# Kernel tuning notes

Hardware: AMD Instinct MI355X
Metric: run time of the kernel (lower is better)

Reference implementation:

```python
import jax, jax.numpy as jnp
import numpy as np
import math

T_STEPS = 100      # diffusion steps
TED = 16           # time_embed_dim
NODE_C = 4         # node_num_classes
EDGE_C = 2         # edge_num_classes
HID = 64           # hidden_dim
H = 4              # nhead
B = 256            # graphs per batch
NPG = 64           # nodes per graph
DEG = 8            # avg out-degree
N = B * NPG
E = N * DEG
IN_CH = NODE_C + TED  # 20


def sinusoidal_embedding(t_vec, dim):
    # t_vec: [1] float. Matches get_sinusoidal_embedding for even dim.
    half = dim // 2
    scale = math.log(10000.0) / (half - 1)
    freqs = jnp.exp(-jnp.arange(half, dtype=jnp.float32) * scale)  # [half]
    emb = t_vec[:, None] * freqs[None, :]                          # [1, half]
    return jnp.concatenate([jnp.sin(emb), jnp.cos(emb)], axis=1)   # [1, dim]


def transformer_conv(x, src, dst, Wq, bq, Wk, bk, Wv, bv, Ws, bs):
    # PyG TransformerConv, concat=False (mean over heads), root_weight=True,
    # beta=False, no edge features, dropout=0 (eval).
    n = x.shape[0]
    q = (x @ Wq + bq).reshape(n, H, HID)
    k = (x @ Wk + bk).reshape(n, H, HID)
    v = (x @ Wv + bv).reshape(n, H, HID)
    # attention logits per edge, softmax over incoming edges of each dst node
    logits = jnp.sum(q[dst] * k[src], axis=-1) / math.sqrt(HID)    # [E, H]
    lmax = jax.ops.segment_max(logits, dst, num_segments=n)       # [n, H]
    ex = jnp.exp(logits - lmax[dst])                              # [E, H]
    denom = jax.ops.segment_sum(ex, dst, num_segments=n)          # [n, H]
    attn = ex / jnp.where(denom == 0, 1.0, denom)[dst]            # [E, H]
    msg = v[src] * attn[:, :, None]                               # [E, H, HID]
    agg = jax.ops.segment_sum(msg, dst, num_segments=n)           # [n, H, HID]
    return agg.mean(axis=1) + x @ Ws + bs                         # [n, HID]


def setup_inputs() -> dict:
    key = jax.random.key(0)
    ks = jax.random.split(key, 32)

    # node features: random one-hot labels
    labels = jax.random.randint(ks[0], (N,), 0, NODE_C)
    x = jax.nn.one_hot(labels, NODE_C, dtype=jnp.float32)

    # per-graph random edges (kept within each graph via offsets)
    src_l = jax.random.randint(ks[1], (B, NPG * DEG), 0, NPG)
    dst_l = jax.random.randint(ks[2], (B, NPG * DEG), 0, NPG)
    off = (jnp.arange(B) * NPG)[:, None]
    edge_index = jnp.stack([(src_l + off).reshape(-1), (dst_l + off).reshape(-1)]).astype(jnp.int64)

    batch = jnp.repeat(jnp.arange(B, dtype=jnp.int64), NPG)

    def lin(k, fin, fout):
        kw, kb = jax.random.split(k)
        W = jax.random.normal(kw, (fin, fout), jnp.float32) / math.sqrt(fin)
        b = jax.random.normal(kb, (fout,), jnp.float32) * 0.01
        return W, b

    W_time, b_time = lin(ks[3], TED, TED)
    Wq1, bq1 = lin(ks[4], IN_CH, H * HID)
    Wk1, bk1 = lin(ks[5], IN_CH, H * HID)
    Wv1, bv1 = lin(ks[6], IN_CH, H * HID)
    Ws1, bs1 = lin(ks[7], IN_CH, HID)
    Wq2, bq2 = lin(ks[8], HID, H * HID)
    Wk2, bk2 = lin(ks[9], HID, H * HID)
    Wv2, bv2 = lin(ks[10], HID, H * HID)
    Ws2, bs2 = lin(ks[11], HID, HID)
    W_node, b_node = lin(ks[12], HID, NODE_C)
    W_e1, b_e1 = lin(ks[13], 2 * HID, HID)
    W_e2, b_e2 = lin(ks[14], HID, EDGE_C)

    return dict(x=x, edge_index=edge_index, batch=batch, t=50,
                W_time=W_time, b_time=b_time,
                Wq1=Wq1, bq1=bq1, Wk1=Wk1, bk1=bk1, Wv1=Wv1, bv1=bv1, Ws1=Ws1, bs1=bs1,
                Wq2=Wq2, bq2=bq2, Wk2=Wk2, bk2=bk2, Wv2=Wv2, bv2=bv2, Ws2=Ws2, bs2=bs2,
                W_node=W_node, b_node=b_node, W_e1=W_e1, b_e1=b_e1, W_e2=W_e2, b_e2=b_e2)


def reference(x, edge_index, batch, t,
              W_time, b_time,
              Wq1, bq1, Wk1, bk1, Wv1, bv1, Ws1, bs1,
              Wq2, bq2, Wk2, bk2, Wv2, bv2, Ws2, bs2,
              W_node, b_node, W_e1, b_e1, W_e2, b_e2):
    src, dst = edge_index[0], edge_index[1]

    # time embedding: sinusoidal(t/T) -> Linear -> broadcast to all nodes
    t_vec = jnp.asarray([t], jnp.float32) / T_STEPS
    temb = sinusoidal_embedding(t_vec, TED) @ W_time + b_time      # [1, TED]
    temb = jnp.broadcast_to(temb, (x.shape[0], TED))
    x_in = jnp.concatenate([x, temb], axis=1)                      # [N, 20]

    h = jax.nn.relu(transformer_conv(x_in, src, dst, Wq1, bq1, Wk1, bk1, Wv1, bv1, Ws1, bs1))
    h = jax.nn.relu(transformer_conv(h, src, dst, Wq2, bq2, Wk2, bk2, Wv2, bv2, Ws2, bs2))

    node_logits = h @ W_node + b_node                              # [N, 4]

    # to_dense_batch with equal-sized graphs == reshape; vectorized edge MLP
    hd = h.reshape(B, NPG, HID)
    pair = jnp.concatenate([
        jnp.broadcast_to(hd[:, :, None, :], (B, NPG, NPG, HID)),
        jnp.broadcast_to(hd[:, None, :, :], (B, NPG, NPG, HID)),
    ], axis=-1)                                                    # [B, n, n, 2*HID]
    e_hidden = jax.nn.relu(pair @ W_e1 + b_e1)
    edge_logits = e_hidden @ W_e2 + b_e2                           # [B, n, n, 2]
    return node_logits, edge_logits
```

## Files before the change

kernel.cpp:

```cpp
#include <hip/hip_runtime.h>
#include <math.h>

constexpr int EPG  = 512;
constexpr int ETOT = 131072;

constexpr size_t TAB_Q  = 0;
constexpr size_t TAB_K  = 1024;
constexpr size_t TAB_V  = 2048;
constexpr size_t TAB_S  = 3072;
constexpr size_t TAB_LG = 3328;
constexpr size_t OFF_H2 = 65536;
constexpr int PK_Q_HI   = 0;
constexpr int PK_Q_LO   = 16384;
constexpr int PK_K_HI   = 32768;
constexpr int PK_K_LO   = 49152;
constexpr int PK_V_HI   = 65536;
constexpr int PK_V_LO   = 81920;
constexpr int PK_S_HI   = 98304;
constexpr int PK_S_LO   = 102400;
constexpr int PK_E1T_HI = 106496;
constexpr int PK_E1T_LO = 110592;
constexpr int PK_E1B_HI = 114688;
constexpr int PK_E1B_LO = 118784;

typedef short bf16x8 __attribute__((ext_vector_type(8)));
typedef float f32x4  __attribute__((ext_vector_type(4)));

__device__ __forceinline__ short f2bf(float x) {
    unsigned u = __float_as_uint(x);
    u = (u + 0x7fffu + ((u >> 16) & 1u)) >> 16;
    return (short)u;
}
__device__ __forceinline__ float bf2f(short h) {
    return __uint_as_float(((unsigned)(unsigned short)h) << 16);
}
__device__ __forceinline__ void splt(float x, short& hi, short& lo) {
    hi = f2bf(x);
    lo = f2bf(x - bf2f(hi));
}

__device__ __forceinline__ f32x4 mfma3(bf16x8 ah, bf16x8 al, bf16x8 bh, bf16x8 bl, f32x4 c) {
    c = __builtin_amdgcn_mfma_f32_16x16x32_bf16(ah, bh, c, 0, 0, 0);
    c = __builtin_amdgcn_mfma_f32_16x16x32_bf16(ah, bl, c, 0, 0, 0);
    c = __builtin_amdgcn_mfma_f32_16x16x32_bf16(al, bh, c, 0, 0, 0);
    return c;
}

__device__ __forceinline__ bf16x8 ldsfrag(const short* p, int rowb, int kb, int lane) {
    return *(const bf16x8*)&p[(rowb + (lane & 15)) * 72 + kb + ((lane >> 4) << 3)];
}
__device__ __forceinline__ bf16x8 gpfrag(const short* p, int colb, int kb, int lane) {
    return *(const bf16x8*)&p[((colb + (lane & 15)) << 6) + kb + ((lane >> 4) << 3)];
}

__device__ __forceinline__ void unpack8(const unsigned* p, bf16x8& hv, bf16x8& lv) {
    uint4 a = *(const uint4*)p;
    uint4 b = *(const uint4*)(p + 4);
    unsigned u[8] = {a.x, a.y, a.z, a.w, b.x, b.y, b.z, b.w};
    bf16x8 h, l;
    #pragma unroll
    for (int i = 0; i < 8; i++) { h[i] = (short)(u[i] >> 16); l[i] = (short)(u[i] & 0xffffu); }
    hv = h; lv = l;
}

__global__ __launch_bounds__(256) void k_tabprep(
    const int* __restrict__ t_ptr,
    const float* __restrict__ Wt,  const float* __restrict__ bt,
    const float* __restrict__ Wq1, const float* __restrict__ bq1,
    const float* __restrict__ Wk1, const float* __restrict__ bk1,
    const float* __restrict__ Wv1, const float* __restrict__ bv1,
    const float* __restrict__ Ws1, const float* __restrict__ bs1,
    const float* __restrict__ Wq2, const float* __restrict__ Wk2,
    const float* __restrict__ Wv2, const float* __restrict__ Ws2,
    const float* __restrict__ We1,
    float* __restrict__ ws, short* __restrict__ wsh)
{
    const int t = threadIdx.x;
    if (blockIdx.x < 240) {
        int b = blockIdx.x;
        const float* src; int N; int dhi; int nb;
        if (b < 64)       { src = Wq2;           N = 256; dhi = PK_Q_HI;   nb = b; }
        else if (b < 128) { src = Wk2;           N = 256; dhi = PK_K_HI;   nb = b - 64; }
        else if (b < 192) { src = Wv2;           N = 256; dhi = PK_V_HI;   nb = b - 128; }
        else if (b < 208) { src = Ws2;           N = 64;  dhi = PK_S_HI;   nb = b - 192; }
        else if (b < 224) { src = We1;           N = 64;  dhi = PK_E1T_HI; nb = b - 208; }
        else              { src = We1 + 64 * 64; N = 64;  dhi = PK_E1B_HI; nb = b - 224; }
        int dlo = dhi + N * 64;
        int n = nb * 4 + (t >> 6), kk = t & 63;
        float v = src[(size_t)kk * N + n];
        short hi, lo; splt(v, hi, lo);
        wsh[dhi + n * 64 + kk] = hi;
        wsh[dlo + n * 64 + kk] = lo;
        return;
    }
    __shared__ float se[16], temb[16];
    __shared__ float q1t[4][256], k1t[4][256], v1t[4][256], s1t[4][64];
    if (t < 8) {
        float tv = (float)(*t_ptr) * 0.01f;
        float scale = logf(10000.0f) / 7.0f;
        float e = tv * expf(-(float)t * scale);
        se[t]     = sinf(e);
        se[t + 8] = cosf(e);
    }
    __syncthreads();
    if (t < 16) {
        float acc = bt[t];
        for (int i = 0; i < 16; i++) acc += se[i] * Wt[i * 16 + t];
        temb[t] = acc;
    }
    __syncthreads();
    {
        const int o = t;
        float tq = 0.f, tk = 0.f, tv = 0.f;
        for (int d = 0; d < 16; d++) {
            float td = temb[d];
            tq += td * Wq1[(4 + d) * 256 + o];
            tk += td * Wk1[(4 + d) * 256 + o];
            tv += td * Wv1[(4 + d) * 256 + o];
        }
        for (int c = 0; c < 4; c++) {
            q1t[c][o] = Wq1[c * 256 + o] + tq + bq1[o];
            k1t[c][o] = Wk1[c * 256 + o] + tk + bk1[o];
            v1t[c][o] = Wv1[c * 256 + o] + tv + bv1[o];
        }
        if (o < 64) {
            float ts = 0.f;
            for (int d = 0; d < 16; d++) ts += temb[d] * Ws1[(4 + d) * 64 + o];
            for (int c = 0; c < 4; c++) s1t[c][o] = Ws1[c * 64 + o] + ts + bs1[o];
        }
    }
    __syncthreads();
    for (int idx = t; idx < 1024; idx += 256) {
        int c = idx >> 8, o = idx & 255;
        ws[TAB_Q + idx] = q1t[c][o];
        ws[TAB_K + idx] = k1t[c][o];
        ws[TAB_V + idx] = v1t[c][o];
    }
    ws[TAB_S + t] = s1t[t >> 6][t & 63];
    if (t < 64) {
        int cd = t >> 4, cs = (t >> 2) & 3, h = t & 3;
        float acc = 0.f;
        for (int d = 0; d < 64; d++) acc += q1t[cd][h * 64 + d] * k1t[cs][h * 64 + d];
        ws[TAB_LG + t] = acc * 0.125f;
    }
}

__global__ __launch_bounds__(512, 4) void k_main(
    const float* __restrict__ x, const int* __restrict__ ei,
    const float* __restrict__ ws, const short* __restrict__ wsh,
    const float* __restrict__ bq, const float* __restrict__ bk,
    const float* __restrict__ bv, const float* __restrict__ bsk,
    float* __restrict__ h2out)
{
    __shared__ __align__(16) char smem[78976];
    short* hHi  = (short*)(smem);
    short* hLo  = (short*)(smem + 9216);
    short* kHi  = (short*)(smem + 18432);
    short* kLo  = (short*)(smem + 27648);
    short* vtHi = (short*)(smem + 36864);
    short* vtLo = (short*)(smem + 46080);
    short* qHi  = (short*)(smem + 55296);
    short* qLo  = (short*)(smem + 59904);
    float* SPf  = (float*)(smem + 64512);
    unsigned* SPu = (unsigned*)(smem + 64512);
    int*   Cc   = (int*)(smem + 73216);
    int*   cnt4 = (int*)(smem + 77312);
    int*   cls  = (int*)(smem + 78336);
    float* lgs  = (float*)(smem + 78592);
    float* invs = (float*)(smem + 78848);
    float* v1t    = (float*)(smem + 18432);
    float* s1t    = (float*)(smem + 22528);
    float* alphaF = (float*)(smem + 23552);

    const int g   = blockIdx.x >> 1;
    const int r0  = (blockIdx.x & 1) * 32;
    const int t   = threadIdx.x;
    const int lane = t & 63, w = t >> 6;
    const int rowbF = (w & 3) * 16;
    const int chF   = w >> 2;
    const int rbQ   = (w & 1) * 16;
    const int cqQ   = (w >> 1) * 16;
    const int lg4   = ((lane >> 4) << 2);
    const int l15   = lane & 15;
    const int row8  = t >> 3;
    const int d08   = (t & 7) * 8;

    for (int i = t; i < 1024; i += 512) v1t[i] = ws[TAB_V + i];
    if (t < 256) s1t[t] = ws[TAB_S + t];
    if (t < 64)  lgs[t] = ws[TAB_LG + t];
    if (t < 64) {
        const float* xr = x + (size_t)(g * 64 + t) * 4;
        int c = 0;
        if (xr[1] > 0.5f) c = 1;
        if (xr[2] > 0.5f) c = 2;
        if (xr[3] > 0.5f) c = 3;
        cls[t] = c;
    }
    if (t < 256) cnt4[t] = 0;
    for (int i = t; i < 1024; i += 512) Cc[i] = 0;
    __syncthreads();

    {
        int ge = g * EPG + t;
        int ls = ei[ge] - g * 64;
        int ld = ei[ETOT + ge] - g * 64;
        atomicAdd(&cnt4[ld * 4 + cls[ls]], 1);
        int lr = ld - r0;
        if ((unsigned)lr < 32u) {
            int idx = lr * 64 + ls;
            atomicAdd(&Cc[idx >> 1], 1 << ((idx & 1) * 16));
        }
    }
    __syncthreads();

    if (t < 256) {
        int n = t >> 2, h = t & 3;
        int cd = cls[n];
        int   c[4]; float l[4];
        #pragma unroll
        for (int cc = 0; cc < 4; cc++) {
            c[cc] = cnt4[n * 4 + cc];
            l[cc] = lgs[cd * 16 + cc * 4 + h];
        }
        float m = -1e30f;
        #pragma unroll
        for (int cc = 0; cc < 4; cc++) if (c[cc] > 0) m = fmaxf(m, l[cc]);
        float e[4]; float den = 0.f;
        #pragma unroll
        for (int cc = 0; cc < 4; cc++) {
            e[cc] = (c[cc] > 0) ? (float)c[cc] * expf(l[cc] - m) : 0.f;
            den += e[cc];
        }
        float inv = (den > 0.f) ? 0.25f / den : 0.f;
        #pragma unroll
        for (int cc = 0; cc < 4; cc++) alphaF[n * 16 + h * 4 + cc] = e[cc] * inv;
    }
    __syncthreads();

    {
        int cd = cls[row8];
        float a[16];
        #pragma unroll
        for (int q = 0; q < 16; q++) a[q] = alphaF[row8 * 16 + q];
        #pragma unroll
        for (int jj = 0; jj < 8; jj++) {
            int d = d08 + jj;
            float acc = s1t[cd * 64 + d];
            #pragma unroll
            for (int h = 0; h < 4; h++)
                #pragma unroll
                for (int c = 0; c < 4; c++)
                    acc += a[h * 4 + c] * v1t[c * 256 + h * 64 + d];
            float o = fmaxf(acc, 0.f);
            short hi, lo; splt(o, hi, lo);
            hHi[row8 * 72 + d] = hi;
            hLo[row8 * 72 + d] = lo;
        }
    }
    __syncthreads();

    bf16x8 AhF0 = ldsfrag(hHi, rowbF, 0, lane),     AhF1 = ldsfrag(hHi, rowbF, 32, lane);
    bf16x8 AlF0 = ldsfrag(hLo, rowbF, 0, lane),     AlF1 = ldsfrag(hLo, rowbF, 32, lane);
    bf16x8 AhQ0 = ldsfrag(hHi, r0 + rbQ, 0, lane),  AhQ1 = ldsfrag(hHi, r0 + rbQ, 32, lane);
    bf16x8 AlQ0 = ldsfrag(hLo, r0 + rbQ, 0, lane),  AlQ1 = ldsfrag(hLo, r0 + rbQ, 32, lane);

    f32x4 skacc;
    {
        f32x4 a = {0.f, 0.f, 0.f, 0.f};
        a = mfma3(AhQ0, AlQ0, gpfrag(wsh + PK_S_HI, cqQ, 0, lane),
                               gpfrag(wsh + PK_S_LO, cqQ, 0, lane), a);
        a = mfma3(AhQ1, AlQ1, gpfrag(wsh + PK_S_HI, cqQ, 32, lane),
                               gpfrag(wsh + PK_S_LO, cqQ, 32, lane), a);
        float bb = bsk[cqQ + l15];
        #pragma unroll
        for (int r = 0; r < 4; r++) a[r] += bb;
        skacc = a;
    }

    float hacc[4] = {0.f, 0.f, 0.f, 0.f};
    #pragma unroll 1
    for (int h = 0; h < 4; h++) {
        #pragma unroll
        for (int ct = 0; ct < 2; ct++) {
            int colb = chF * 32 + ct * 16;
            int gcol = h * 64 + colb;
            f32x4 ka = {0.f, 0.f, 0.f, 0.f}, va = {0.f, 0.f, 0.f, 0.f};
            ka = mfma3(AhF0, AlF0, gpfrag(wsh + PK_K_HI, gcol, 0, lane),
                                    gpfrag(wsh + PK_K_LO, gcol, 0, lane), ka);
            ka = mfma3(AhF1, AlF1, gpfrag(wsh + PK_K_HI, gcol, 32, lane),
                                    gpfrag(wsh + PK_K_LO, gcol, 32, lane), ka);
            va = mfma3(AhF0, AlF0, gpfrag(wsh + PK_V_HI, gcol, 0, lane),
                                    gpfrag(wsh + PK_V_LO, gcol, 0, lane), va);
            va = mfma3(AhF1, AlF1, gpfrag(wsh + PK_V_HI, gcol, 32, lane),
                                    gpfrag(wsh + PK_V_LO, gcol, 32, lane), va);
            float bkv = bk[gcol + l15];
            float bvv = bv[gcol + l15];
            int cc = colb + l15;
            #pragma unroll
            for (int r = 0; r < 4; r++) {
                int rr = rowbF + lg4 + r;
                short hi, lo;
                splt(ka[r] + bkv, hi, lo);
                kHi[rr * 72 + cc] = hi;  kLo[rr * 72 + cc] = lo;
                splt(va[r] + bvv, hi, lo);
                vtHi[cc * 72 + rr] = hi; vtLo[cc * 72 + rr] = lo;
            }
        }
        {
            int gcol = h * 64 + cqQ;
            f32x4 qa = {0.f, 0.f, 0.f, 0.f};
            qa = mfma3(AhQ0, AlQ0, gpfrag(wsh + PK_Q_HI, gcol, 0, lane),
                                    gpfrag(wsh + PK_Q_LO, gcol, 0, lane), qa);
            qa = mfma3(AhQ1, AlQ1, gpfrag(wsh + PK_Q_HI, gcol, 32, lane),
                                    gpfrag(wsh + PK_Q_LO, gcol, 32, lane), qa);
            float bqv = bq[gcol + l15];
            int cc = cqQ + l15;
            #pragma unroll
            for (int r = 0; r < 4; r++) {
                int rr = rbQ + lg4 + r;
                short hi, lo;
                splt((qa[r] + bqv) * 0.125f, hi, lo);
                qHi[rr * 72 + cc] = hi;  qLo[rr * 72 + cc] = lo;
            }
        }
        __syncthreads();

        {
            bf16x8 qh0 = ldsfrag(qHi, rbQ, 0, lane),  qh1 = ldsfrag(qHi, rbQ, 32, lane);
            bf16x8 ql0 = ldsfrag(qLo, rbQ, 0, lane),  ql1 = ldsfrag(qLo, rbQ, 32, lane);
            f32x4 s = {0.f, 0.f, 0.f, 0.f};
            s = mfma3(qh0, ql0, ldsfrag(kHi, cqQ, 0, lane),
                                 ldsfrag(kLo, cqQ, 0, lane), s);
            s = mfma3(qh1, ql1, ldsfrag(kHi, cqQ, 32, lane),
                                 ldsfrag(kLo, cqQ, 32, lane), s);
            int cc = cqQ + l15;
            #pragma unroll
            for (int r = 0; r < 4; r++)
                SPf[(rbQ + lg4 + r) * 68 + cc] = s[r];
        }
        __syncthreads();

        if (t < 256) {
            int row = t >> 3, c8 = (t & 7) * 8;
            float4 s0 = *(float4*)&SPf[row * 68 + c8];
            float4 s1 = *(float4*)&SPf[row * 68 + c8 + 4];
            float sv[8] = {s0.x, s0.y, s0.z, s0.w, s1.x, s1.y, s1.z, s1.w};
            int cv[8];
            #pragma unroll
            for (int jj = 0; jj < 8; jj++) {
                int idx = row * 64 + c8 + jj;
                cv[jj] = (Cc[idx >> 1] >> ((idx & 1) * 16)) & 0xffff;
            }
            float m = -1e30f;
            #pragma unroll
            for (int jj = 0; jj < 8; jj++) if (cv[jj] > 0) m = fmaxf(m, sv[jj]);
            m = fmaxf(m, __shfl_xor(m, 1, 8));
            m = fmaxf(m, __shfl_xor(m, 2, 8));
            m = fmaxf(m, __shfl_xor(m, 4, 8));
            float den = 0.f; float p[8];
            #pragma unroll
            for (int jj = 0; jj < 8; jj++) {
                p[jj] = (cv[jj] > 0) ? (float)cv[jj] * expf(sv[jj] - m) : 0.f;
                den += p[jj];
            }
            den += __shfl_xor(den, 1, 8);
            den += __shfl_xor(den, 2, 8);
            den += __shfl_xor(den, 4, 8);
            #pragma unroll
            for (int jj = 0; jj < 8; jj++) {
                short hi, lo; splt(p[jj], hi, lo);
                SPu[row * 68 + c8 + jj] =
                    ((unsigned)(unsigned short)hi << 16) | (unsigned short)lo;
            }
            if ((t & 7) == 0) invs[row] = (den > 0.f) ? 1.f / den : 0.f;
        }
        __syncthreads();

        {
            bf16x8 ph0, pl0, ph1, pl1;
            const unsigned* pp = SPu + (rbQ + l15) * 68 + ((lane >> 4) << 3);
            unpack8(pp, ph0, pl0);
            unpack8(pp + 32, ph1, pl1);
            f32x4 pv = {0.f, 0.f, 0.f, 0.f};
            pv = mfma3(ph0, pl0, ldsfrag(vtHi, cqQ, 0, lane),
                                  ldsfrag(vtLo, cqQ, 0, lane), pv);
            pv = mfma3(ph1, pl1, ldsfrag(vtHi, cqQ, 32, lane),
                                  ldsfrag(vtLo, cqQ, 32, lane), pv);
            #pragma unroll
            for (int r = 0; r < 4; r++)
                hacc[r] += pv[r] * invs[rbQ + lg4 + r];
        }
        __syncthreads();
    }

    {
        int cc = cqQ + l15;
        #pragma unroll
        for (int r = 0; r < 4; r++) {
            int lr = rbQ + lg4 + r;
            float v = fmaxf(0.25f * hacc[r] + skacc[r], 0.f);
            h2out[(size_t)(g * 64 + r0 + lr) * 64 + cc] = v;
        }
    }
}

__global__ __launch_bounds__(512, 4) void k_edge(
    const short* __restrict__ wsh, const float* __restrict__ h2g,
    const float* __restrict__ Wn, const float* __restrict__ bn,
    const float* __restrict__ be1, const float* __restrict__ We2,
    const float* __restrict__ be2, float* __restrict__ out)
{
    __shared__ __align__(16) char smem[46080];
    short* h2Hi = (short*)(smem);
    short* h2Lo = (short*)(smem + 9216);
    float* Af   = (float*)(smem + 18432);
    float* BTf  = (float*)(smem + 27136);
    float* WnS  = (float*)(smem + 44544);
    float* w2s  = (float*)(smem + 45568);

    const int g  = blockIdx.x >> 1;
    const int r0 = (blockIdx.x & 1) * 32;
    const int t  = threadIdx.x;
    const int lane = t & 63, w = t >> 6;
    const int rowbF = (w & 3) * 16, chF = w >> 2;
    const int rbQ = (w & 1) * 16,   cqQ = (w >> 1) * 16;
    const int lg4 = ((lane >> 4) << 2);
    const int l15 = lane & 15;

    {
        int row = t >> 3, c8 = (t & 7) * 8;
        float4 a = *(const float4*)&h2g[(size_t)(g * 64 + row) * 64 + c8];
        float4 b = *(const float4*)&h2g[(size_t)(g * 64 + row) * 64 + c8 + 4];
        float vv[8] = {a.x, a.y, a.z, a.w, b.x, b.y, b.z, b.w};
        #pragma unroll
        for (int i = 0; i < 8; i++) {
            short hi, lo; splt(vv[i], hi, lo);
            h2Hi[row * 72 + c8 + i] = hi;
            h2Lo[row * 72 + c8 + i] = lo;
        }
    }
    if (t < 256) WnS[t] = Wn[t];
    if (t < 128) w2s[(t & 1) * 64 + (t >> 1)] = We2[t];
    __syncthreads();

    {
        bf16x8 aq0 = ldsfrag(h2Hi, r0 + rbQ, 0, lane), aq1 = ldsfrag(h2Hi, r0 + rbQ, 32, lane);
        bf16x8 lq0 = ldsfrag(h2Lo, r0 + rbQ, 0, lane), lq1 = ldsfrag(h2Lo, r0 + rbQ, 32, lane);
        f32x4 aa = {0.f, 0.f, 0.f, 0.f};
        aa = mfma3(aq0, lq0, gpfrag(wsh + PK_E1T_HI, cqQ, 0, lane),
                              gpfrag(wsh + PK_E1T_LO, cqQ, 0, lane), aa);
        aa = mfma3(aq1, lq1, gpfrag(wsh + PK_E1T_HI, cqQ, 32, lane),
                              gpfrag(wsh + PK_E1T_LO, cqQ, 32, lane), aa);
        float bev = be1[cqQ + l15];
        #pragma unroll
        for (int r = 0; r < 4; r++)
            Af[(rbQ + lg4 + r) * 68 + cqQ + l15] = aa[r] + bev;

        bf16x8 af0 = ldsfrag(h2Hi, rowbF, 0, lane), af1 = ldsfrag(h2Hi, rowbF, 32, lane);
        bf16x8 lf0 = ldsfrag(h2Lo, rowbF, 0, lane), lf1 = ldsfrag(h2Lo, rowbF, 32, lane);
        #pragma unroll
        for (int ct = 0; ct < 2; ct++) {
            int colb = chF * 32 + ct * 16;
            f32x4 bb = {0.f, 0.f, 0.f, 0.f};
            bb = mfma3(af0, lf0, gpfrag(wsh + PK_E1B_HI, colb, 0, lane),
                                  gpfrag(wsh + PK_E1B_LO, colb, 0, lane), bb);
            bb = mfma3(af1, lf1, gpfrag(wsh + PK_E1B_HI, colb, 32, lane),
                                  gpfrag(wsh + PK_E1B_LO, colb, 32, lane), bb);
            int cc = colb + l15;
            #pragma unroll
            for (int r = 0; r < 4; r++)
                BTf[cc * 68 + rowbF + lg4 + r] = bb[r];
        }
    }
    if (t < 128) {
        int n = t >> 2, c = t & 3;
        float acc = bn[c];
        #pragma unroll 4
        for (int k = 0; k < 64; k++)
            acc += (bf2f(h2Hi[(r0 + n) * 72 + k]) + bf2f(h2Lo[(r0 + n) * 72 + k])) * WnS[k * 4 + c];
        out[(size_t)(g * 64 + r0 + n) * 4 + c] = acc;
    }
    __syncthreads();

    {
        const int wv = t >> 6, j = t & 63;
        float e0[4], e1[4];
        const float cb0 = be2[0], cb1 = be2[1];
        #pragma unroll
        for (int ii = 0; ii < 4; ii++) { e0[ii] = cb0; e1[ii] = cb1; }
        for (int kb = 0; kb < 4; kb++) {
            const int k0 = kb * 16;
            float bj[16], wa[16], wb[16];
            #pragma unroll
            for (int q = 0; q < 16; q++) {
                bj[q] = BTf[(k0 + q) * 68 + j];
                wa[q] = w2s[k0 + q];
                wb[q] = w2s[64 + k0 + q];
            }
            #pragma unroll
            for (int ii = 0; ii < 4; ii++) {
                const float* ar = &Af[(wv * 4 + ii) * 68 + k0];
                #pragma unroll
                for (int q = 0; q < 16; q += 4) {
                    float4 a4 = *(const float4*)(ar + q);
                    float s;
                    s = fmaxf(a4.x + bj[q + 0], 0.f); e0[ii] += s * wa[q + 0]; e1[ii] += s * wb[q + 0];
                    s = fmaxf(a4.y + bj[q + 1], 0.f); e0[ii] += s * wa[q + 1]; e1[ii] += s * wb[q + 1];
                    s = fmaxf(a4.z + bj[q + 2], 0.f); e0[ii] += s * wa[q + 2]; e1[ii] += s * wb[q + 2];
                    s = fmaxf(a4.w + bj[q + 3], 0.f); e0[ii] += s * wa[q + 3]; e1[ii] += s * wb[q + 3];
                }
            }
        }
        float2* oe = (float2*)(out + 65536);
        #pragma unroll
        for (int ii = 0; ii < 4; ii++)
            oe[(size_t)(g * 64 + r0 + wv * 4 + ii) * 64 + j] = make_float2(e0[ii], e1[ii]);
    }
}

extern "C" void kernel_launch(void* const* d_in, const int* in_sizes, int n_in,
                              void* d_out, int out_size, void* d_ws, size_t ws_size,
                              hipStream_t stream)
{
    const float* x    = (const float*)d_in[0];
    const int*   ei   = (const int*)d_in[1];
    const int*   tptr = (const int*)d_in[3];
    const float* Wt   = (const float*)d_in[4];
    const float* bt   = (const float*)d_in[5];
    const float* Wq1  = (const float*)d_in[6];
    const float* bq1  = (const float*)d_in[7];
    const float* Wk1  = (const float*)d_in[8];
    const float* bk1  = (const float*)d_in[9];
    const float* Wv1  = (const float*)d_in[10];
    const float* bv1  = (const float*)d_in[11];
    const float* Ws1  = (const float*)d_in[12];
    const float* bs1  = (const float*)d_in[13];
    const float* Wq2  = (const float*)d_in[14];
    const float* bq2  = (const float*)d_in[15];
    const float* Wk2  = (const float*)d_in[16];
    const float* bk2  = (const float*)d_in[17];
    const float* Wv2  = (const float*)d_in[18];
    const float* bv2  = (const float*)d_in[19];
    const float* Ws2  = (const float*)d_in[20];
    const float* bs2  = (const float*)d_in[21];
    const float* Wn   = (const float*)d_in[22];
    const float* bn   = (const float*)d_in[23];
    const float* We1  = (const float*)d_in[24];
    const float* be1  = (const float*)d_in[25];
    const float* We2  = (const float*)d_in[26];
    const float* be2  = (const float*)d_in[27];

    float* ws  = (float*)d_ws;
    short* wsh = (short*)(ws + 4096);
    float* h2  = ws + OFF_H2;
    float* out = (float*)d_out;

    k_tabprep<<<241, 256, 0, stream>>>(tptr, Wt, bt, Wq1, bq1, Wk1, bk1, Wv1, bv1,
                                       Ws1, bs1, Wq2, Wk2, Wv2, Ws2, We1, ws, wsh);
    k_main<<<512, 512, 0, stream>>>(x, ei, ws, wsh, bq2, bk2, bv2, bs2, h2);
    k_edge<<<512, 512, 0, stream>>>(wsh, h2, Wn, bn, be1, We2, be2, out);
}
```

Measured before the change: 76.29 us.

## Fold Wq·Wkᵀ into a per-head bilinear matrix and pass h2 as packed bf16 pairs

Layer-2 attention logits are now computed as (h·M_h)·hᵀ, where M_h = Wq_h·Wk_hᵀ/8 is precomputed per head in the prep kernel. Because the key bias only adds a per-row constant, which softmax cancels, it is dropped, and the query-bias term folds into a per-column vector. This removes the per-block K projection and lets the softmax run on MFMA fragments in registers, cutting LDS traffic and shared memory. h2 is stored as packed hi/lo bf16 words so the edge kernel no longer has to re-split it, and expf is swapped for __expf, at some risk to accuracy.

```diff
diff --git a/kernel.cpp b/kernel.cpp
--- a/kernel.cpp
+++ b/kernel.cpp
@@ -9,19 +9,19 @@
 constexpr size_t TAB_V  = 2048;
 constexpr size_t TAB_S  = 3072;
 constexpr size_t TAB_LG = 3328;
-constexpr size_t OFF_H2 = 65536;
-constexpr int PK_Q_HI   = 0;
-constexpr int PK_Q_LO   = 16384;
-constexpr int PK_K_HI   = 32768;
-constexpr int PK_K_LO   = 49152;
-constexpr int PK_V_HI   = 65536;
-constexpr int PK_V_LO   = 81920;
-constexpr int PK_S_HI   = 98304;
-constexpr int PK_S_LO   = 102400;
-constexpr int PK_E1T_HI = 106496;
-constexpr int PK_E1T_LO = 110592;
-constexpr int PK_E1B_HI = 114688;
-constexpr int PK_E1B_LO = 118784;
+constexpr size_t TAB_VV = 3392;
+constexpr size_t OFF_H2P = 65536;
+
+constexpr int PK_V_HI   = 0;
+constexpr int PK_V_LO   = 16384;
+constexpr int PK_S_HI   = 32768;
+constexpr int PK_S_LO   = 36864;
+constexpr int PK_E1T_HI = 40960;
+constexpr int PK_E1T_LO = 45056;
+constexpr int PK_E1B_HI = 49152;
+constexpr int PK_E1B_LO = 53248;
+constexpr int PK_M_HI   = 57344;
+constexpr int PK_M_LO   = 73728;
 
 typedef short bf16x8 __attribute__((ext_vector_type(8)));
 typedef float f32x4  __attribute__((ext_vector_type(4)));
@@ -70,27 +70,49 @@
     const float* __restrict__ Wk1, const float* __restrict__ bk1,
     const float* __restrict__ Wv1, const float* __restrict__ bv1,
     const float* __restrict__ Ws1, const float* __restrict__ bs1,
-    const float* __restrict__ Wq2, const float* __restrict__ Wk2,
-    const float* __restrict__ Wv2, const float* __restrict__ Ws2,
-    const float* __restrict__ We1,
+    const float* __restrict__ Wq2, const float* __restrict__ bq2,
+    const float* __restrict__ Wk2, const float* __restrict__ Wv2,
+    const float* __restrict__ Ws2, const float* __restrict__ We1,
     float* __restrict__ ws, short* __restrict__ wsh)
 {
-    const int t = threadIdx.x;
-    if (blockIdx.x < 240) {
-        int b = blockIdx.x;
+    const int t = threadIdx.x, b = blockIdx.x;
+    if (b < 112) {
         const float* src; int N; int dhi; int nb;
-        if (b < 64)       { src = Wq2;           N = 256; dhi = PK_Q_HI;   nb = b; }
-        else if (b < 128) { src = Wk2;           N = 256; dhi = PK_K_HI;   nb = b - 64; }
-        else if (b < 192) { src = Wv2;           N = 256; dhi = PK_V_HI;   nb = b - 128; }
-        else if (b < 208) { src = Ws2;           N = 64;  dhi = PK_S_HI;   nb = b - 192; }
-        else if (b < 224) { src = We1;           N = 64;  dhi = PK_E1T_HI; nb = b - 208; }
-        else              { src = We1 + 64 * 64; N = 64;  dhi = PK_E1B_HI; nb = b - 224; }
+        if (b < 64)      { src = Wv2;           N = 256; dhi = PK_V_HI;   nb = b; }
+        else if (b < 80) { src = Ws2;           N = 64;  dhi = PK_S_HI;   nb = b - 64; }
+        else if (b < 96) { src = We1;           N = 64;  dhi = PK_E1T_HI; nb = b - 80; }
+        else             { src = We1 + 64 * 64; N = 64;  dhi = PK_E1B_HI; nb = b - 96; }
         int dlo = dhi + N * 64;
         int n = nb * 4 + (t >> 6), kk = t & 63;
         float v = src[(size_t)kk * N + n];
         short hi, lo; splt(v, hi, lo);
         wsh[dhi + n * 64 + kk] = hi;
         wsh[dlo + n * 64 + kk] = lo;
+        return;
+    }
+    if (b < 116) {
+        int h = b - 112;
+        __shared__ float wq[64][65], wk[64][65];
+        for (int i = t; i < 4096; i += 256) {
+            int r = i >> 6, a = i & 63;
+            wq[r][a] = Wq2[(size_t)r * 256 + h * 64 + a];
+            wk[r][a] = Wk2[(size_t)r * 256 + h * 64 + a];
+        }
+        __syncthreads();
+        int m = t >> 2, k0 = (t & 3) * 16;
+        for (int kk = k0; kk < k0 + 16; kk++) {
+            float acc = 0.f;
+            for (int a = 0; a < 64; a++) acc += wq[kk][a] * wk[m][a];
+            acc *= 0.125f;
+            short hi, lo; splt(acc, hi, lo);
+            wsh[PK_M_HI + h * 4096 + m * 64 + kk] = hi;
+            wsh[PK_M_LO + h * 4096 + m * 64 + kk] = lo;
+        }
+        if (t < 64) {
+            float acc = 0.f;
+            for (int a = 0; a < 64; a++) acc += wk[t][a] * bq2[h * 64 + a];
+            ws[TAB_VV + h * 64 + t] = 0.125f * acc;
+        }
         return;
     }
     __shared__ float se[16], temb[16];
@@ -148,46 +170,45 @@
 __global__ __launch_bounds__(512, 4) void k_main(
     const float* __restrict__ x, const int* __restrict__ ei,
     const float* __restrict__ ws, const short* __restrict__ wsh,
-    const float* __restrict__ bq, const float* __restrict__ bk,
     const float* __restrict__ bv, const float* __restrict__ bsk,
-    float* __restrict__ h2out)
+    unsigned* __restrict__ h2p)
 {
-    __shared__ __align__(16) char smem[78976];
+    __shared__ __align__(16) char smem[61184];
     short* hHi  = (short*)(smem);
     short* hLo  = (short*)(smem + 9216);
-    short* kHi  = (short*)(smem + 18432);
-    short* kLo  = (short*)(smem + 27648);
-    short* vtHi = (short*)(smem + 36864);
-    short* vtLo = (short*)(smem + 46080);
-    short* qHi  = (short*)(smem + 55296);
-    short* qLo  = (short*)(smem + 59904);
-    float* SPf  = (float*)(smem + 64512);
-    unsigned* SPu = (unsigned*)(smem + 64512);
-    int*   Cc   = (int*)(smem + 73216);
-    int*   cnt4 = (int*)(smem + 77312);
-    int*   cls  = (int*)(smem + 78336);
-    float* lgs  = (float*)(smem + 78592);
-    float* invs = (float*)(smem + 78848);
-    float* v1t    = (float*)(smem + 18432);
-    float* s1t    = (float*)(smem + 22528);
-    float* alphaF = (float*)(smem + 23552);
+    short* GHi  = (short*)(smem + 18432);
+    short* GLo  = (short*)(smem + 23040);
+    short* VtHi = (short*)(smem + 27648);
+    short* VtLo = (short*)(smem + 36864);
+    float* SPf  = (float*)(smem + 46080);
+    int*   Cc   = (int*)(smem + 54784);
+    float* wcol = (float*)(smem + 59136);
+    float* vvs  = (float*)(smem + 60160);
+    float* v1t    = (float*)(smem + 27648);
+    float* s1t    = (float*)(smem + 31744);
+    float* lgs    = (float*)(smem + 32768);
+    float* alphaF = (float*)(smem + 33024);
+    int*   cls    = (int*)(smem + 37120);
+    int*   cnt4   = (int*)(smem + 37376);
 
     const int g   = blockIdx.x >> 1;
     const int r0  = (blockIdx.x & 1) * 32;
     const int t   = threadIdx.x;
     const int lane = t & 63, w = t >> 6;
-    const int rowbF = (w & 3) * 16;
-    const int chF   = w >> 2;
-    const int rbQ   = (w & 1) * 16;
-    const int cqQ   = (w >> 1) * 16;
-    const int lg4   = ((lane >> 4) << 2);
-    const int l15   = lane & 15;
-    const int row8  = t >> 3;
-    const int d08   = (t & 7) * 8;
+    const int rb  = (w & 1) * 16;
+    const int cb  = (w >> 1) * 16;
+    const int db  = (w & 3) * 16;
+    const int jb0 = (w >> 2) * 32;
+    const int lg4 = ((lane >> 4) << 2);
+    const int lg8 = ((lane >> 4) << 3);
+    const int l15 = lane & 15;
+    const int row8 = t >> 3;
+    const int d08  = (t & 7) * 8;
 
     for (int i = t; i < 1024; i += 512) v1t[i] = ws[TAB_V + i];
     if (t < 256) s1t[t] = ws[TAB_S + t];
     if (t < 64)  lgs[t] = ws[TAB_LG + t];
+    if (t < 256) vvs[t] = ws[TAB_VV + t];
     if (t < 64) {
         const float* xr = x + (size_t)(g * 64 + t) * 4;
         int c = 0;
@@ -197,7 +218,7 @@
         cls[t] = c;
     }
     if (t < 256) cnt4[t] = 0;
-    for (int i = t; i < 1024; i += 512) Cc[i] = 0;
+    for (int i = t; i < 1056; i += 512) Cc[i] = 0;
     __syncthreads();
 
     {
@@ -207,7 +228,7 @@
         atomicAdd(&cnt4[ld * 4 + cls[ls]], 1);
         int lr = ld - r0;
         if ((unsigned)lr < 32u) {
-            int idx = lr * 64 + ls;
+            int idx = lr * 66 + ls;
             atomicAdd(&Cc[idx >> 1], 1 << ((idx & 1) * 16));
         }
     }
@@ -228,7 +249,7 @@
         float e[4]; float den = 0.f;
         #pragma unroll
         for (int cc = 0; cc < 4; cc++) {
-            e[cc] = (c[cc] > 0) ? (float)c[cc] * expf(l[cc] - m) : 0.f;
+            e[cc] = (c[cc] > 0) ? (float)c[cc] * __expf(l[cc] - m) : 0.f;
             den += e[cc];
         }
         float inv = (den > 0.f) ? 0.25f / den : 0.f;
@@ -259,164 +280,169 @@
     }
     __syncthreads();
 
-    bf16x8 AhF0 = ldsfrag(hHi, rowbF, 0, lane),     AhF1 = ldsfrag(hHi, rowbF, 32, lane);
-    bf16x8 AlF0 = ldsfrag(hLo, rowbF, 0, lane),     AlF1 = ldsfrag(hLo, rowbF, 32, lane);
-    bf16x8 AhQ0 = ldsfrag(hHi, r0 + rbQ, 0, lane),  AhQ1 = ldsfrag(hHi, r0 + rbQ, 32, lane);
-    bf16x8 AlQ0 = ldsfrag(hLo, r0 + rbQ, 0, lane),  AlQ1 = ldsfrag(hLo, r0 + rbQ, 32, lane);
-
-    f32x4 skacc;
-    {
-        f32x4 a = {0.f, 0.f, 0.f, 0.f};
-        a = mfma3(AhQ0, AlQ0, gpfrag(wsh + PK_S_HI, cqQ, 0, lane),
-                               gpfrag(wsh + PK_S_LO, cqQ, 0, lane), a);
-        a = mfma3(AhQ1, AlQ1, gpfrag(wsh + PK_S_HI, cqQ, 32, lane),
-                               gpfrag(wsh + PK_S_LO, cqQ, 32, lane), a);
-        float bb = bsk[cqQ + l15];
-        #pragma unroll
-        for (int r = 0; r < 4; r++) a[r] += bb;
-        skacc = a;
+    bf16x8 AhQ0 = ldsfrag(hHi, r0 + rb, 0, lane),  AhQ1 = ldsfrag(hHi, r0 + rb, 32, lane);
+    bf16x8 AlQ0 = ldsfrag(hLo, r0 + rb, 0, lane),  AlQ1 = ldsfrag(hLo, r0 + rb, 32, lane);
+    bf16x8 sb0h = ldsfrag(hHi, cb, 0, lane),  sb0l = ldsfrag(hLo, cb, 0, lane);
+    bf16x8 sb1h = ldsfrag(hHi, cb, 32, lane), sb1l = ldsfrag(hLo, cb, 32, lane);
+
+    if (t < 256) {
+        int j = t >> 2, hh = t & 3;
+        float acc = 0.f;
+        #pragma unroll 8
+        for (int k = 0; k < 64; k++)
+            acc += (bf2f(hHi[j * 72 + k]) + bf2f(hLo[j * 72 + k])) * vvs[hh * 64 + k];
+        wcol[hh * 64 + j] = acc;
+    }
+
+    f32x4 skacc = {0.f, 0.f, 0.f, 0.f};
+    {
+        bf16x8 s0h = gpfrag(wsh + PK_S_HI, cb, 0, lane),  s0l = gpfrag(wsh + PK_S_LO, cb, 0, lane);
+        bf16x8 s1h = gpfrag(wsh + PK_S_HI, cb, 32, lane), s1l = gpfrag(wsh + PK_S_LO, cb, 32, lane);
+        skacc = mfma3(AhQ0, AlQ0, s0h, s0l, skacc);
+        skacc = mfma3(AhQ1, AlQ1, s1h, s1l, skacc);
+        float bb = bsk[cb + l15];
+        #pragma unroll
+        for (int r = 0; r < 4; r++) skacc[r] += bb;
     }
 
     float hacc[4] = {0.f, 0.f, 0.f, 0.f};
     #pragma unroll 1
     for (int h = 0; h < 4; h++) {
-        #pragma unroll
-        for (int ct = 0; ct < 2; ct++) {
-            int colb = chF * 32 + ct * 16;
-            int gcol = h * 64 + colb;
-            f32x4 ka = {0.f, 0.f, 0.f, 0.f}, va = {0.f, 0.f, 0.f, 0.f};
-            ka = mfma3(AhF0, AlF0, gpfrag(wsh + PK_K_HI, gcol, 0, lane),
-                                    gpfrag(wsh + PK_K_LO, gcol, 0, lane), ka);
-            ka = mfma3(AhF1, AlF1, gpfrag(wsh + PK_K_HI, gcol, 32, lane),
-                                    gpfrag(wsh + PK_K_LO, gcol, 32, lane), ka);
-            va = mfma3(AhF0, AlF0, gpfrag(wsh + PK_V_HI, gcol, 0, lane),
-                                    gpfrag(wsh + PK_V_LO, gcol, 0, lane), va);
-            va = mfma3(AhF1, AlF1, gpfrag(wsh + PK_V_HI, gcol, 32, lane),
-                                    gpfrag(wsh + PK_V_LO, gcol, 32, lane), va);
-            float bkv = bk[gcol + l15];
-            float bvv = bv[gcol + l15];
-            int cc = colb + l15;
+        const short* pmh = wsh + PK_M_HI + h * 4096;
+        const short* pml = wsh + PK_M_LO + h * 4096;
+        bf16x8 m0h = gpfrag(pmh, cb, 0, lane),  m0l = gpfrag(pml, cb, 0, lane);
+        bf16x8 m1h = gpfrag(pmh, cb, 32, lane), m1l = gpfrag(pml, cb, 32, lane);
+        int gc0 = h * 64 + db;
+        bf16x8 va0h = gpfrag(wsh + PK_V_HI, gc0, 0, lane),  va0l = gpfrag(wsh + PK_V_LO, gc0, 0, lane);
+        bf16x8 va1h = gpfrag(wsh + PK_V_HI, gc0, 32, lane), va1l = gpfrag(wsh + PK_V_LO, gc0, 32, lane);
+        float4 bv4 = *(const float4*)&bv[gc0 + lg4];
+        bf16x8 hb00 = ldsfrag(hHi, jb0, 0, lane),       hb00l = ldsfrag(hLo, jb0, 0, lane);
+        bf16x8 hb01 = ldsfrag(hHi, jb0, 32, lane),      hb01l = ldsfrag(hLo, jb0, 32, lane);
+        bf16x8 hb10 = ldsfrag(hHi, jb0 + 16, 0, lane),  hb10l = ldsfrag(hLo, jb0 + 16, 0, lane);
+        bf16x8 hb11 = ldsfrag(hHi, jb0 + 16, 32, lane), hb11l = ldsfrag(hLo, jb0 + 16, 32, lane);
+
+        {
+            f32x4 ga = {0.f, 0.f, 0.f, 0.f};
+            ga = mfma3(AhQ0, AlQ0, m0h, m0l, ga);
+            ga = mfma3(AhQ1, AlQ1, m1h, m1l, ga);
+            int cc = cb + l15;
             #pragma unroll
             for (int r = 0; r < 4; r++) {
-                int rr = rowbF + lg4 + r;
+                short hi, lo; splt(ga[r], hi, lo);
+                GHi[(rb + lg4 + r) * 72 + cc] = hi;
+                GLo[(rb + lg4 + r) * 72 + cc] = lo;
+            }
+        }
+        {
+            f32x4 vt0 = {0.f, 0.f, 0.f, 0.f}, vt1 = {0.f, 0.f, 0.f, 0.f};
+            vt0 = mfma3(va0h, va0l, hb00, hb00l, vt0);
+            vt0 = mfma3(va1h, va1l, hb01, hb01l, vt0);
+            vt1 = mfma3(va0h, va0l, hb10, hb10l, vt1);
+            vt1 = mfma3(va1h, va1l, hb11, hb11l, vt1);
+            #pragma unroll
+            for (int r = 0; r < 4; r++) {
+                int rr = (db + lg4 + r) * 72;
                 short hi, lo;
-                splt(ka[r] + bkv, hi, lo);
-                kHi[rr * 72 + cc] = hi;  kLo[rr * 72 + cc] = lo;
-                splt(va[r] + bvv, hi, lo);
-                vtHi[cc * 72 + rr] = hi; vtLo[cc * 72 + rr] = lo;
-            }
-        }
+                splt(vt0[r] + bv4[r], hi, lo);
+                VtHi[rr + jb0 + l15] = hi;      VtLo[rr + jb0 + l15] = lo;
+                splt(vt1[r] + bv4[r], hi, lo);
+                VtHi[rr + jb0 + 16 + l15] = hi; VtLo[rr + jb0 + 16 + l15] = lo;
+            }
+        }
+        __syncthreads();
+
+        bf16x8 vb0h = ldsfrag(VtHi, cb, 0, lane),  vb0l = ldsfrag(VtLo, cb, 0, lane);
+        bf16x8 vb1h = ldsfrag(VtHi, cb, 32, lane), vb1l = ldsfrag(VtLo, cb, 32, lane);
         {
-            int gcol = h * 64 + cqQ;
-            f32x4 qa = {0.f, 0.f, 0.f, 0.f};
-            qa = mfma3(AhQ0, AlQ0, gpfrag(wsh + PK_Q_HI, gcol, 0, lane),
-                                    gpfrag(wsh + PK_Q_LO, gcol, 0, lane), qa);
-            qa = mfma3(AhQ1, AlQ1, gpfrag(wsh + PK_Q_HI, gcol, 32, lane),
-                                    gpfrag(wsh + PK_Q_LO, gcol, 32, lane), qa);
-            float bqv = bq[gcol + l15];
-            int cc = cqQ + l15;
-            #pragma unroll
-            for (int r = 0; r < 4; r++) {
-                int rr = rbQ + lg4 + r;
+            bf16x8 g0h = ldsfrag(GHi, rb, 0, lane),  g0l = ldsfrag(GLo, rb, 0, lane);
+            bf16x8 g1h = ldsfrag(GHi, rb, 32, lane), g1l = ldsfrag(GLo, rb, 32, lane);
+            f32x4 s = {0.f, 0.f, 0.f, 0.f};
+            s = mfma3(g0h, g0l, sb0h, sb0l, s);
+            s = mfma3(g1h, g1l, sb1h, sb1l, s);
+            int cc = cb + l15;
+            #pragma unroll
+            for (int r = 0; r < 4; r++)
+                SPf[(rb + lg4 + r) * 68 + cc] = s[r];
+        }
+        __syncthreads();
+
+        {
+            const int lr = rb + l15;
+            float sv[16];
+            {
+                float4 a0 = *(const float4*)&SPf[lr * 68 + lg8];
+                float4 a1 = *(const float4*)&SPf[lr * 68 + lg8 + 4];
+                float4 a2 = *(const float4*)&SPf[lr * 68 + 32 + lg8];
+                float4 a3 = *(const float4*)&SPf[lr * 68 + 32 + lg8 + 4];
+                sv[0]=a0.x; sv[1]=a0.y; sv[2]=a0.z; sv[3]=a0.w;
+                sv[4]=a1.x; sv[5]=a1.y; sv[6]=a1.z; sv[7]=a1.w;
+                sv[8]=a2.x; sv[9]=a2.y; sv[10]=a2.z; sv[11]=a2.w;
+                sv[12]=a3.x; sv[13]=a3.y; sv[14]=a3.z; sv[15]=a3.w;
+            }
+            int cv[16];
+            #pragma unroll
+            for (int e = 0; e < 8; e++) {
+                int i0 = lr * 66 + lg8 + e;
+                int i1 = lr * 66 + 32 + lg8 + e;
+                cv[e]     = (Cc[i0 >> 1] >> ((i0 & 1) * 16)) & 0xffff;
+                cv[8 + e] = (Cc[i1 >> 1] >> ((i1 & 1) * 16)) & 0xffff;
+                sv[e]     += wcol[h * 64 + lg8 + e];
+                sv[8 + e] += wcol[h * 64 + 32 + lg8 + e];
+            }
+            float m = -1e30f;
+            #pragma unroll
+            for (int e = 0; e < 16; e++) if (cv[e] > 0) m = fmaxf(m, sv[e]);
+            m = fmaxf(m, __shfl_xor(m, 16));
+            m = fmaxf(m, __shfl_xor(m, 32));
+            float den = 0.f; float p[16];
+            #pragma unroll
+            for (int e = 0; e < 16; e++) {
+                p[e] = (cv[e] > 0) ? (float)cv[e] * __expf(sv[e] - m) : 0.f;
+                den += p[e];
+            }
+            den += __shfl_xor(den, 16);
+            den += __shfl_xor(den, 32);
+            float inv = (den > 0.f) ? 1.f / den : 0.f;
+            bf16x8 pa0h, pa0l, pa1h, pa1l;
+            #pragma unroll
+            for (int e = 0; e < 8; e++) {
                 short hi, lo;
-                splt((qa[r] + bqv) * 0.125f, hi, lo);
-                qHi[rr * 72 + cc] = hi;  qLo[rr * 72 + cc] = lo;
-            }
+                splt(p[e] * inv, hi, lo);      pa0h[e] = hi; pa0l[e] = lo;
+                splt(p[8 + e] * inv, hi, lo);  pa1h[e] = hi; pa1l[e] = lo;
+            }
+            f32x4 pv = {0.f, 0.f, 0.f, 0.f};
+            pv = mfma3(pa0h, pa0l, vb0h, vb0l, pv);
+            pv = mfma3(pa1h, pa1l, vb1h, vb1l, pv);
+            #pragma unroll
+            for (int r = 0; r < 4; r++) hacc[r] += pv[r];
         }
         __syncthreads();
-
-        {
-            bf16x8 qh0 = ldsfrag(qHi, rbQ, 0, lane),  qh1 = ldsfrag(qHi, rbQ, 32, lane);
-            bf16x8 ql0 = ldsfrag(qLo, rbQ, 0, lane),  ql1 = ldsfrag(qLo, rbQ, 32, lane);
-            f32x4 s = {0.f, 0.f, 0.f, 0.f};
-            s = mfma3(qh0, ql0, ldsfrag(kHi, cqQ, 0, lane),
-                                 ldsfrag(kLo, cqQ, 0, lane), s);
-            s = mfma3(qh1, ql1, ldsfrag(kHi, cqQ, 32, lane),
-                                 ldsfrag(kLo, cqQ, 32, lane), s);
-            int cc = cqQ + l15;
-            #pragma unroll
-            for (int r = 0; r < 4; r++)
-                SPf[(rbQ + lg4 + r) * 68 + cc] = s[r];
-        }
-        __syncthreads();
-
-        if (t < 256) {
-            int row = t >> 3, c8 = (t & 7) * 8;
-            float4 s0 = *(float4*)&SPf[row * 68 + c8];
-            float4 s1 = *(float4*)&SPf[row * 68 + c8 + 4];
-            float sv[8] = {s0.x, s0.y, s0.z, s0.w, s1.x, s1.y, s1.z, s1.w};
-            int cv[8];
-            #pragma unroll
-            for (int jj = 0; jj < 8; jj++) {
-                int idx = row * 64 + c8 + jj;
-                cv[jj] = (Cc[idx >> 1] >> ((idx & 1) * 16)) & 0xffff;
-            }
-            float m = -1e30f;
-            #pragma unroll
-            for (int jj = 0; jj < 8; jj++) if (cv[jj] > 0) m = fmaxf(m, sv[jj]);
-            m = fmaxf(m, __shfl_xor(m, 1, 8));
-            m = fmaxf(m, __shfl_xor(m, 2, 8));
-            m = fmaxf(m, __shfl_xor(m, 4, 8));
-            float den = 0.f; float p[8];
-            #pragma unroll
-            for (int jj = 0; jj < 8; jj++) {
-                p[jj] = (cv[jj] > 0) ? (float)cv[jj] * expf(sv[jj] - m) : 0.f;
-                den += p[jj];
-            }
-            den += __shfl_xor(den, 1, 8);
-            den += __shfl_xor(den, 2, 8);
-            den += __shfl_xor(den, 4, 8);
-            #pragma unroll
-            for (int jj = 0; jj < 8; jj++) {
-                short hi, lo; splt(p[jj], hi, lo);
-                SPu[row * 68 + c8 + jj] =
-                    ((unsigned)(unsigned short)hi << 16) | (unsigned short)lo;
-            }
-            if ((t & 7) == 0) invs[row] = (den > 0.f) ? 1.f / den : 0.f;
-        }
-        __syncthreads();
-
-        {
-            bf16x8 ph0, pl0, ph1, pl1;
-            const unsigned* pp = SPu + (rbQ + l15) * 68 + ((lane >> 4) << 3);
-            unpack8(pp, ph0, pl0);
-            unpack8(pp + 32, ph1, pl1);
-            f32x4 pv = {0.f, 0.f, 0.f, 0.f};
-            pv = mfma3(ph0, pl0, ldsfrag(vtHi, cqQ, 0, lane),
-                                  ldsfrag(vtLo, cqQ, 0, lane), pv);
-            pv = mfma3(ph1, pl1, ldsfrag(vtHi, cqQ, 32, lane),
-                                  ldsfrag(vtLo, cqQ, 32, lane), pv);
-            #pragma unroll
-            for (int r = 0; r < 4; r++)
-                hacc[r] += pv[r] * invs[rbQ + lg4 + r];
-        }
-        __syncthreads();
-    }
-
-    {
-        int cc = cqQ + l15;
+    }
+
+    {
+        int cc = cb + l15;
         #pragma unroll
         for (int r = 0; r < 4; r++) {
-            int lr = rbQ + lg4 + r;
             float v = fmaxf(0.25f * hacc[r] + skacc[r], 0.f);
-            h2out[(size_t)(g * 64 + r0 + lr) * 64 + cc] = v;
+            short hi, lo; splt(v, hi, lo);
+            unsigned u = ((unsigned)(unsigned short)hi << 16) | (unsigned short)(unsigned short)lo;
+            h2p[(size_t)(g * 64 + r0 + rb + lg4 + r) * 64 + cc] = u;
         }
     }
 }
 
 __global__ __launch_bounds__(512, 4) void k_edge(
-    const short* __restrict__ wsh, const float* __restrict__ h2g,
+    const short* __restrict__ wsh, const unsigned* __restrict__ h2g,
     const float* __restrict__ Wn, const float* __restrict__ bn,
     const float* __restrict__ be1, const float* __restrict__ We2,
     const float* __restrict__ be2, float* __restrict__ out)
 {
-    __shared__ __align__(16) char smem[46080];
-    short* h2Hi = (short*)(smem);
-    short* h2Lo = (short*)(smem + 9216);
-    float* Af   = (float*)(smem + 18432);
-    float* BTf  = (float*)(smem + 27136);
-    float* WnS  = (float*)(smem + 44544);
-    float* w2s  = (float*)(smem + 45568);
+    __shared__ __align__(16) char smem[45056];
+    unsigned* h2P = (unsigned*)(smem);
+    float* Af   = (float*)(smem + 17408);
+    float* BTf  = (float*)(smem + 26112);
+    float* WnS  = (float*)(smem + 43520);
+    float* w2s  = (float*)(smem + 44544);
 
     const int g  = blockIdx.x >> 1;
     const int r0 = (blockIdx.x & 1) * 32;
@@ -425,47 +451,46 @@
     const int rowbF = (w & 3) * 16, chF = w >> 2;
     const int rbQ = (w & 1) * 16,   cqQ = (w >> 1) * 16;
     const int lg4 = ((lane >> 4) << 2);
+    const int lg8 = ((lane >> 4) << 3);
     const int l15 = lane & 15;
 
     {
         int row = t >> 3, c8 = (t & 7) * 8;
-        float4 a = *(const float4*)&h2g[(size_t)(g * 64 + row) * 64 + c8];
-        float4 b = *(const float4*)&h2g[(size_t)(g * 64 + row) * 64 + c8 + 4];
-        float vv[8] = {a.x, a.y, a.z, a.w, b.x, b.y, b.z, b.w};
-        #pragma unroll
-        for (int i = 0; i < 8; i++) {
-            short hi, lo; splt(vv[i], hi, lo);
-            h2Hi[row * 72 + c8 + i] = hi;
-            h2Lo[row * 72 + c8 + i] = lo;
-        }
+        uint4 a = *(const uint4*)&h2g[(size_t)(g * 64 + row) * 64 + c8];
+        uint4 b = *(const uint4*)&h2g[(size_t)(g * 64 + row) * 64 + c8 + 4];
+        *(uint4*)&h2P[row * 68 + c8]     = a;
+        *(uint4*)&h2P[row * 68 + c8 + 4] = b;
     }
     if (t < 256) WnS[t] = Wn[t];
     if (t < 128) w2s[(t & 1) * 64 + (t >> 1)] = We2[t];
     __syncthreads();
 
     {
-        bf16x8 aq0 = ldsfrag(h2Hi, r0 + rbQ, 0, lane), aq1 = ldsfrag(h2Hi, r0 + rbQ, 32, lane);
-        bf16x8 lq0 = ldsfrag(h2Lo, r0 + rbQ, 0, lane), lq1 = ldsfrag(h2Lo, r0 + rbQ, 32, lane);
+        bf16x8 e0h = gpfrag(wsh + PK_E1T_HI, cqQ, 0, lane),  e0l = gpfrag(wsh + PK_E1T_LO, cqQ, 0, lane);
+        bf16x8 e1h = gpfrag(wsh + PK_E1T_HI, cqQ, 32, lane), e1l = gpfrag(wsh + PK_E1T_LO, cqQ, 32, lane);
+        bf16x8 aq0, lq0, aq1, lq1;
+        unpack8(&h2P[(r0 + rbQ + l15) * 68 + lg8], aq0, lq0);
+        unpack8(&h2P[(r0 + rbQ + l15) * 68 + 32 + lg8], aq1, lq1);
         f32x4 aa = {0.f, 0.f, 0.f, 0.f};
-        aa = mfma3(aq0, lq0, gpfrag(wsh + PK_E1T_HI, cqQ, 0, lane),
-                              gpfrag(wsh + PK_E1T_LO, cqQ, 0, lane), aa);
-        aa = mfma3(aq1, lq1, gpfrag(wsh + PK_E1T_HI, cqQ, 32, lane),
-                              gpfrag(wsh + PK_E1T_LO, cqQ, 32, lane), aa);
+        aa = mfma3(aq0, lq0, e0h, e0l, aa);
+        aa = mfma3(aq1, lq1, e1h, e1l, aa);
         float bev = be1[cqQ + l15];
         #pragma unroll
         for (int r = 0; r < 4; r++)
             Af[(rbQ + lg4 + r) * 68 + cqQ + l15] = aa[r] + bev;
-
-        bf16x8 af0 = ldsfrag(h2Hi, rowbF, 0, lane), af1 = ldsfrag(h2Hi, rowbF, 32, lane);
-        bf16x8 lf0 = ldsfrag(h2Lo, rowbF, 0, lane), lf1 = ldsfrag(h2Lo, rowbF, 32, lane);
+    }
+    {
+        bf16x8 af0, lf0, af1, lf1;
+        unpack8(&h2P[(rowbF + l15) * 68 + lg8], af0, lf0);
+        unpack8(&h2P[(rowbF + l15) * 68 + 32 + lg8], af1, lf1);
         #pragma unroll
         for (int ct = 0; ct < 2; ct++) {
             int colb = chF * 32 + ct * 16;
+            bf16x8 b0h = gpfrag(wsh + PK_E1B_HI, colb, 0, lane),  b0l = gpfrag(wsh + PK_E1B_LO, colb, 0, lane);
+            bf16x8 b1h = gpfrag(wsh + PK_E1B_HI, colb, 32, lane), b1l = gpfrag(wsh + PK_E1B_LO, colb, 32, lane);
             f32x4 bb = {0.f, 0.f, 0.f, 0.f};
-            bb = mfma3(af0, lf0, gpfrag(wsh + PK_E1B_HI, colb, 0, lane),
-                                  gpfrag(wsh + PK_E1B_LO, colb, 0, lane), bb);
-            bb = mfma3(af1, lf1, gpfrag(wsh + PK_E1B_HI, colb, 32, lane),
-                                  gpfrag(wsh + PK_E1B_LO, colb, 32, lane), bb);
+            bb = mfma3(af0, lf0, b0h, b0l, bb);
+            bb = mfma3(af1, lf1, b1h, b1l, bb);
             int cc = colb + l15;
             #pragma unroll
             for (int r = 0; r < 4; r++)
@@ -475,9 +500,12 @@
     if (t < 128) {
         int n = t >> 2, c = t & 3;
         float acc = bn[c];
-        #pragma unroll 4
-        for (int k = 0; k < 64; k++)
-            acc += (bf2f(h2Hi[(r0 + n) * 72 + k]) + bf2f(h2Lo[(r0 + n) * 72 + k])) * WnS[k * 4 + c];
+        #pragma unroll 8
+        for (int k = 0; k < 64; k++) {
+            unsigned u = h2P[(r0 + n) * 68 + k];
+            float val = __uint_as_float(u & 0xffff0000u) + __uint_as_float(u << 16);
+            acc += val * WnS[k * 4 + c];
+        }
         out[(size_t)(g * 64 + r0 + n) * 4 + c] = acc;
     }
     __syncthreads();
@@ -538,7 +566,6 @@
     const float* Wq2  = (const float*)d_in[14];
     const float* bq2  = (const float*)d_in[15];
     const float* Wk2  = (const float*)d_in[16];
-    const float* bk2  = (const float*)d_in[17];
     const float* Wv2  = (const float*)d_in[18];
     const float* bv2  = (const float*)d_in[19];
     const float* Ws2  = (const float*)d_in[20];
@@ -552,11 +579,11 @@
 
     float* ws  = (float*)d_ws;
     short* wsh = (short*)(ws + 4096);
-    float* h2  = ws + OFF_H2;
+    unsigned* h2p = (unsigned*)(ws + OFF_H2P);
     float* out = (float*)d_out;
 
-    k_tabprep<<<241, 256, 0, stream>>>(tptr, Wt, bt, Wq1, bq1, Wk1, bk1, Wv1, bv1,
-                                       Ws1, bs1, Wq2, Wk2, Wv2, Ws2, We1, ws, wsh);
-    k_main<<<512, 512, 0, stream>>>(x, ei, ws, wsh, bq2, bk2, bv2, bs2, h2);
-    k_edge<<<512, 512, 0, stream>>>(wsh, h2, Wn, bn, be1, We2, be2, out);
-}
+    k_tabprep<<<117, 256, 0, stream>>>(tptr, Wt, bt, Wq1, bq1, Wk1, bk1, Wv1, bv1,
+                                       Ws1, bs1, Wq2, bq2, Wk2, Wv2, Ws2, We1, ws, wsh);
+    k_main<<<512, 512, 0, stream>>>(x, ei, ws, wsh, bv2, bs2, h2p);
+    k_edge<<<512, 512, 0, stream>>>(wsh, h2p, Wn, bn, be1, We2, be2, out);
+}
```

Measured after the change: 65.82 us. -13.7%, faster.
